# Kernel tuning notes

Hardware: AMD Instinct MI355X
Metric: run time of the kernel (lower is better)

## Reference

```python
import jax, jax.numpy as jnp
import numpy as np

B, T = 512, 200
N_SKILLS, M, DK, DV, H = 1000, 50, 64, 64, 128


def setup_inputs() -> dict:
    key = jax.random.key(0)
    ks = jax.random.split(key, 12)
    inp = {
        'skill_seq': jax.random.randint(ks[0], (B, T), 0, N_SKILLS, dtype=jnp.int32),
        'correct_seq': jax.random.randint(ks[1], (B, T), 0, 2, dtype=jnp.int32),
        'mask': jnp.ones((B, T), dtype=jnp.float32),
        'skill_embed': jax.random.normal(ks[2], (N_SKILLS, DK), dtype=jnp.float32),
        'key_memory': jax.random.normal(ks[3], (M, DK), dtype=jnp.float32) * 0.1,
        'value_init': jnp.zeros((M, DV), dtype=jnp.float32),
        'interaction_embed': jax.random.normal(ks[4], (2 * N_SKILLS, DV), dtype=jnp.float32),
        'erase_W': jax.random.normal(ks[5], (DV, DV), dtype=jnp.float32) * 0.05,
        'erase_b': jnp.zeros((DV,), dtype=jnp.float32),
        'add_W': jax.random.normal(ks[6], (DV, DV), dtype=jnp.float32) * 0.05,
        'add_b': jnp.zeros((DV,), dtype=jnp.float32),
        'fc1_W': jax.random.normal(ks[7], (DK + DV, H), dtype=jnp.float32) * 0.05,
        'fc1_b': jnp.zeros((H,), dtype=jnp.float32),
        'fc2_W': jax.random.normal(ks[8], (H, 1), dtype=jnp.float32) * 0.05,
        'fc2_b': jnp.zeros((1,), dtype=jnp.float32),
    }
    return inp


def reference(skill_seq, correct_seq, mask, skill_embed, key_memory, value_init,
              interaction_embed, erase_W, erase_b, add_W, add_b,
              fc1_W, fc1_b, fc2_W, fc2_b):
    n_skills = skill_embed.shape[0]
    b = skill_seq.shape[0]
    # Time-invariant-per-step quantities are precomputed vectorized over (B,T):
    q = skill_embed[skill_seq]                                   # (B,T,dk)
    w = jax.nn.softmax(jnp.einsum('btk,mk->btm', q, key_memory), axis=-1)  # (B,T,M)
    v = interaction_embed[skill_seq + correct_seq * n_skills]    # (B,T,dv)
    e = jax.nn.sigmoid(v @ erase_W + erase_b)                    # (B,T,dv)
    a = jnp.tanh(v @ add_W + add_b)                              # (B,T,dv)

    def step(mem, inputs):
        # mem: (B,M,dv); read BEFORE write, matching the torch loop
        w_t, e_t, a_t = inputs                                   # (B,M),(B,dv),(B,dv)
        read = jnp.einsum('bm,bmv->bv', w_t, mem)                # (B,dv)
        we = w_t[:, :, None]                                     # (B,M,1)
        mem = mem * (1.0 - we * e_t[:, None, :]) + we * a_t[:, None, :]
        return mem, read

    mem0 = jnp.broadcast_to(value_init, (b,) + value_init.shape)
    _, reads = jax.lax.scan(step, mem0,
                            (jnp.swapaxes(w, 0, 1), jnp.swapaxes(e, 0, 1), jnp.swapaxes(a, 0, 1)))
    reads = jnp.swapaxes(reads, 0, 1)                            # (B,T,dv)

    x = jnp.concatenate([q, reads], axis=-1)                     # (B,T,dk+dv)
    h = jax.nn.relu(x @ fc1_W + fc1_b)
    logit = (h @ fc2_W + fc2_b)[..., 0]
    p = jax.nn.sigmoid(logit)
    return p * mask, correct_seq.astype(jnp.float32) * mask
```

## Files before the change

### kernel.cpp

```cpp
#include <hip/hip_runtime.h>
#include <hip/hip_bf16.h>

#define B_  512
#define T_  200
#define NS  1000
#define M_  50
#define DK  64
#define DV  64
#define H_  128
#define NPOS (B_ * T_)

typedef __hip_bfloat16 bf16;
typedef unsigned short ushort_t;
typedef __bf16 bf16x8 __attribute__((ext_vector_type(8)));
typedef float  f32x4  __attribute__((ext_vector_type(4)));

__device__ __forceinline__ float ldf(const void* p, int i, int isbf) {
    return isbf ? __bfloat162float(((const bf16*)p)[i]) : ((const float*)p)[i];
}
__device__ __forceinline__ int sniff(const void* mask) {
    return (*(const unsigned*)mask == 0x3F800000u) ? 0 : 1;
}
__device__ __forceinline__ float rl(float x, int l) {
    return __int_as_float(__builtin_amdgcn_readlane(__float_as_int(x), l));
}
__device__ __forceinline__ ushort_t f2bf(float v) {
    bf16 h = __float2bfloat16(v);
    return *(ushort_t*)&h;
}

__global__ __launch_bounds__(256) void dk16_tabs(
    const void* __restrict__ mask,
    const void* __restrict__ skill_embed, const void* __restrict__ key_memory,
    const void* __restrict__ inter,
    const void* __restrict__ eW, const void* __restrict__ eb,
    const void* __restrict__ aW, const void* __restrict__ ab,
    const void* __restrict__ fc1W, const void* __restrict__ fc1b,
    float* __restrict__ w_tab, unsigned* __restrict__ ea_tab,
    float* __restrict__ hq_tab, ushort_t* __restrict__ W2f) {
    int isbf = sniff(mask);
    int lane = threadIdx.x & 63;
    int gwid = (blockIdx.x << 2) | (threadIdx.x >> 6);

    if (gwid < NS) {
        int s = gwid;
        float q = ldf(skill_embed, s * DK + lane, isbf);
        float acc = 0.f;
        if (lane < M_) {
            #pragma unroll 16
            for (int k = 0; k < DK; ++k)
                acc = fmaf(rl(q, k), ldf(key_memory, lane * DK + k, isbf), acc);
        }
        float val = (lane < M_) ? acc : -1e30f;
        float mx = val;
        #pragma unroll
        for (int off = 1; off < 64; off <<= 1) mx = fmaxf(mx, __shfl_xor(mx, off, 64));
        float ex = (lane < M_) ? __expf(val - mx) : 0.f;
        float sm = ex;
        #pragma unroll
        for (int off = 1; off < 64; off <<= 1) sm += __shfl_xor(sm, off, 64);
        w_tab[s * 64 + lane] = (lane < M_) ? ex / sm : 0.f;
    } else if (gwid < 3 * NS) {
        int r = gwid - NS;
        float vv = ldf(inter, r * DV + lane, isbf);
        float eacc = ldf(eb, lane, isbf);
        float aacc = ldf(ab, lane, isbf);
        #pragma unroll 16
        for (int u = 0; u < DV; ++u) {
            float vu = rl(vv, u);
            eacc = fmaf(vu, ldf(eW, u * DV + lane, isbf), eacc);
            aacc = fmaf(vu, ldf(aW, u * DV + lane, isbf), aacc);
        }
        float ev = 1.f / (1.f + __expf(-eacc));
        float av = tanhf(aacc);
        ea_tab[r * 64 + lane] = ((unsigned)f2bf(av) << 16) | (unsigned)f2bf(ev);
    } else if (gwid < 4 * NS) {
        int s = gwid - 3 * NS;
        float q = ldf(skill_embed, s * DK + lane, isbf);
        float acc0 = ldf(fc1b, lane, isbf);
        float acc1 = ldf(fc1b, 64 + lane, isbf);
        #pragma unroll 16
        for (int k = 0; k < DK; ++k) {
            float qk = rl(q, k);
            acc0 = fmaf(qk, ldf(fc1W, k * H_ + lane, isbf), acc0);
            acc1 = fmaf(qk, ldf(fc1W, k * H_ + 64 + lane, isbf), acc1);
        }
        hq_tab[s * H_ + lane]      = acc0;
        hq_tab[s * H_ + 64 + lane] = acc1;
    } else if (gwid < 4 * NS + 64) {
        int f = gwid - 4 * NS;
        int tile = f >> 3, kk = f & 7;
        int n = tile * 16 + (lane & 15);
        #pragma unroll
        for (int j = 0; j < 8; ++j) {
            int v = (kk * 32 + (lane >> 4) * 8 + j) & 63;
            W2f[(f * 64 + lane) * 8 + j] = f2bf(ldf(fc1W, (DK + v) * H_ + n, isbf));
        }
    }
}

template<int KS>
__global__ __launch_bounds__(64, 2) void dk16_scan(
    const int*  __restrict__ ss, const int* __restrict__ cs,
    const void* __restrict__ mask, const void* __restrict__ value_init,
    const float* __restrict__ w_tab, const unsigned* __restrict__ ea_tab,
    ushort_t* __restrict__ read_bf) {

    constexpr int NW = 16 / KS;
    int isbf = sniff(mask);
    int lane = threadIdx.x;
    int bk   = blockIdx.x;
    int b    = bk / KS, k = bk - b * KS;
    const int base = b * T_;
    const int row0 = (64 / KS) * k;
    const float4* w4 = (const float4*)w_tab;

    float4 mem[NW];
    #pragma unroll
    for (int i = 0; i < NW; ++i) {
        int r = row0 + 4 * i;
        mem[i].x = (r + 0 < M_) ? ldf(value_init, (r + 0) * DV + lane, isbf) : 0.f;
        mem[i].y = (r + 1 < M_) ? ldf(value_init, (r + 1) * DV + lane, isbf) : 0.f;
        mem[i].z = (r + 2 < M_) ? ldf(value_init, (r + 2) * DV + lane, isbf) : 0.f;
        mem[i].w = (r + 3 < M_) ? ldf(value_init, (r + 3) * DV + lane, isbf) : 0.f;
    }

    int s2 = ss[base + 2], c2 = cs[base + 2];
    int s3 = ss[base + 3], c3 = cs[base + 3];

    float4 wa[NW], wb[NW];
    unsigned eaA, eaB;
    {
        int sA = ss[base], cA = cs[base];
        eaA = ea_tab[(sA + cA * NS) * 64 + lane];
        #pragma unroll
        for (int i = 0; i < NW; ++i) wa[i] = w4[sA * 16 + NW * k + i];
        int sB = ss[base + 1], cB = cs[base + 1];
        eaB = ea_tab[(sB + cB * NS) * 64 + lane];
        #pragma unroll
        for (int i = 0; i < NW; ++i) wb[i] = w4[sB * 16 + NW * k + i];
    }

    for (int t = 0; t < T_; t += 2) {
        {
            float e0 = __uint_as_float(eaA << 16);
            float a0 = __uint_as_float(eaA & 0xFFFF0000u);
            float acc0 = 0.f, acc1 = 0.f, acc2 = 0.f, acc3 = 0.f;
            #pragma unroll
            for (int i = 0; i < NW; ++i) {
                float4 w = wa[i];
                acc0 = fmaf(w.x, mem[i].x, acc0);
                acc1 = fmaf(w.y, mem[i].y, acc1);
                acc2 = fmaf(w.z, mem[i].z, acc2);
                acc3 = fmaf(w.w, mem[i].w, acc3);
                mem[i].x = fmaf(-w.x, fmaf(e0, mem[i].x, -a0), mem[i].x);
                mem[i].y = fmaf(-w.y, fmaf(e0, mem[i].y, -a0), mem[i].y);
                mem[i].z = fmaf(-w.z, fmaf(e0, mem[i].z, -a0), mem[i].z);
                mem[i].w = fmaf(-w.w, fmaf(e0, mem[i].w, -a0), mem[i].w);
            }
            read_bf[((size_t)(base + t) * KS + k) * 64 + lane] =
                f2bf((acc0 + acc1) + (acc2 + acc3));
        }
        {
            eaA = ea_tab[(s2 + c2 * NS) * 64 + lane];
            #pragma unroll
            for (int i = 0; i < NW; ++i) wa[i] = w4[s2 * 16 + NW * k + i];
        }
        s2 = s3; c2 = c3;
        int tf = (t + 4 < T_) ? t + 4 : T_ - 1;
        s3 = ss[base + tf]; c3 = cs[base + tf];

        {
            float e1 = __uint_as_float(eaB << 16);
            float a1 = __uint_as_float(eaB & 0xFFFF0000u);
            float acc0 = 0.f, acc1 = 0.f, acc2 = 0.f, acc3 = 0.f;
            #pragma unroll
            for (int i = 0; i < NW; ++i) {
                float4 w = wb[i];
                acc0 = fmaf(w.x, mem[i].x, acc0);
                acc1 = fmaf(w.y, mem[i].y, acc1);
                acc2 = fmaf(w.z, mem[i].z, acc2);
                acc3 = fmaf(w.w, mem[i].w, acc3);
                mem[i].x = fmaf(-w.x, fmaf(e1, mem[i].x, -a1), mem[i].x);
                mem[i].y = fmaf(-w.y, fmaf(e1, mem[i].y, -a1), mem[i].y);
                mem[i].z = fmaf(-w.z, fmaf(e1, mem[i].z, -a1), mem[i].z);
                mem[i].w = fmaf(-w.w, fmaf(e1, mem[i].w, -a1), mem[i].w);
            }
            read_bf[((size_t)(base + t + 1) * KS + k) * 64 + lane] =
                f2bf((acc0 + acc1) + (acc2 + acc3));
        }
        {
            eaB = ea_tab[(s2 + c2 * NS) * 64 + lane];
            #pragma unroll
            for (int i = 0; i < NW; ++i) wb[i] = w4[s2 * 16 + NW * k + i];
        }
        s2 = s3; c2 = c3;
        tf = (t + 5 < T_) ? t + 5 : T_ - 1;
        s3 = ss[base + tf]; c3 = cs[base + tf];
    }
}

#define FOR8(X) X(0) X(1) X(2) X(3) X(4) X(5) X(6) X(7)
#define DECL_BT(t) bf16x8 b##t##_0, b##t##_1, b##t##_2, b##t##_3, \
                          b##t##_4, b##t##_5, b##t##_6, b##t##_7;
#define LOAD_BT(t) \
    b##t##_0 = B8[((t)*8+0)*64+lane]; b##t##_1 = B8[((t)*8+1)*64+lane]; \
    b##t##_2 = B8[((t)*8+2)*64+lane]; b##t##_3 = B8[((t)*8+3)*64+lane]; \
    b##t##_4 = B8[((t)*8+4)*64+lane]; b##t##_5 = B8[((t)*8+5)*64+lane]; \
    b##t##_6 = B8[((t)*8+6)*64+lane]; b##t##_7 = B8[((t)*8+7)*64+lane];
#define DECL_C(t)  f32x4 c##t = {0.f, 0.f, 0.f, 0.f};
#define LOAD_A(kk) bf16x8 a##kk = A8[col * 32 + (kk) * 4 + quad];
#define MFMA_KK(kk) \
    c0 = __builtin_amdgcn_mfma_f32_16x16x32_bf16(a##kk, b0_##kk, c0, 0, 0, 0); \
    c1 = __builtin_amdgcn_mfma_f32_16x16x32_bf16(a##kk, b1_##kk, c1, 0, 0, 0); \
    c2 = __builtin_amdgcn_mfma_f32_16x16x32_bf16(a##kk, b2_##kk, c2, 0, 0, 0); \
    c3 = __builtin_amdgcn_mfma_f32_16x16x32_bf16(a##kk, b3_##kk, c3, 0, 0, 0); \
    c4 = __builtin_amdgcn_mfma_f32_16x16x32_bf16(a##kk, b4_##kk, c4, 0, 0, 0); \
    c5 = __builtin_amdgcn_mfma_f32_16x16x32_bf16(a##kk, b5_##kk, c5, 0, 0, 0); \
    c6 = __builtin_amdgcn_mfma_f32_16x16x32_bf16(a##kk, b6_##kk, c6, 0, 0, 0); \
    c7 = __builtin_amdgcn_mfma_f32_16x16x32_bf16(a##kk, b7_##kk, c7, 0, 0, 0);
#define EPI(t) { \
    float h; \
    h = c##t.x + hq_tab[s0r * H_ + t * 16 + col]; x0 = fmaf(fmaxf(h, 0.f), f2w##t, x0); \
    h = c##t.y + hq_tab[s1r * H_ + t * 16 + col]; x1 = fmaf(fmaxf(h, 0.f), f2w##t, x1); \
    h = c##t.z + hq_tab[s2r * H_ + t * 16 + col]; x2 = fmaf(fmaxf(h, 0.f), f2w##t, x2); \
    h = c##t.w + hq_tab[s3r * H_ + t * 16 + col]; x3 = fmaf(fmaxf(h, 0.f), f2w##t, x3); }

__global__ __launch_bounds__(64)
__attribute__((amdgpu_waves_per_eu(1))) void dk16_fc4(
    const int*  __restrict__ skill_seq, const int* __restrict__ correct_seq,
    const void* __restrict__ mask,
    const void* __restrict__ fc2W, const void* __restrict__ fc2b,
    const float* __restrict__ hq_tab, const ushort_t* __restrict__ W2f,
    const ushort_t* __restrict__ read_bf,
    float* __restrict__ out0, float* __restrict__ out1) {

    int isbf = sniff(mask);
    int lane = threadIdx.x;
    int col  = lane & 15, quad = lane >> 4;

    const bf16x8* B8 = (const bf16x8*)W2f;
    DECL_BT(0) DECL_BT(1) DECL_BT(2) DECL_BT(3)
    DECL_BT(4) DECL_BT(5) DECL_BT(6) DECL_BT(7)
    FOR8(LOAD_BT)

    float f2w0 = ldf(fc2W,   0 + col, isbf), f2w1 = ldf(fc2W,  16 + col, isbf);
    float f2w2 = ldf(fc2W,  32 + col, isbf), f2w3 = ldf(fc2W,  48 + col, isbf);
    float f2w4 = ldf(fc2W,  64 + col, isbf), f2w5 = ldf(fc2W,  80 + col, isbf);
    float f2w6 = ldf(fc2W,  96 + col, isbf), f2w7 = ldf(fc2W, 112 + col, isbf);
    float f2b  = ldf(fc2b, 0, isbf);

    for (int pg = blockIdx.x; pg < NPOS / 16; pg += gridDim.x) {
        int p0 = pg * 16;
        const bf16x8* A8 = (const bf16x8*)(read_bf + (size_t)p0 * 256);
        LOAD_A(0) LOAD_A(1) LOAD_A(2) LOAD_A(3)
        LOAD_A(4) LOAD_A(5) LOAD_A(6) LOAD_A(7)

        int s0r = skill_seq[p0 + quad * 4 + 0];
        int s1r = skill_seq[p0 + quad * 4 + 1];
        int s2r = skill_seq[p0 + quad * 4 + 2];
        int s3r = skill_seq[p0 + quad * 4 + 3];

        FOR8(DECL_C)
        FOR8(MFMA_KK)

        float x0 = 0.f, x1 = 0.f, x2 = 0.f, x3 = 0.f;
        FOR8(EPI)

        #pragma unroll
        for (int off = 1; off < 16; off <<= 1) {
            x0 += __shfl_xor(x0, off, 64);
            x1 += __shfl_xor(x1, off, 64);
            x2 += __shfl_xor(x2, off, 64);
            x3 += __shfl_xor(x3, off, 64);
        }

        float mk0 = ldf(mask, p0 + quad * 4 + 0, isbf);
        float mk1 = ldf(mask, p0 + quad * 4 + 1, isbf);
        float mk2 = ldf(mask, p0 + quad * 4 + 2, isbf);
        float mk3 = ldf(mask, p0 + quad * 4 + 3, isbf);
        if (col == 0) {
            out0[p0 + quad * 4 + 0] = mk0 / (1.f + __expf(-(x0 + f2b)));
            out0[p0 + quad * 4 + 1] = mk1 / (1.f + __expf(-(x1 + f2b)));
            out0[p0 + quad * 4 + 2] = mk2 / (1.f + __expf(-(x2 + f2b)));
            out0[p0 + quad * 4 + 3] = mk3 / (1.f + __expf(-(x3 + f2b)));
        }
        if (col == 1) {
            out1[p0 + quad * 4 + 0] = (float)correct_seq[p0 + quad * 4 + 0] * mk0;
            out1[p0 + quad * 4 + 1] = (float)correct_seq[p0 + quad * 4 + 1] * mk1;
            out1[p0 + quad * 4 + 2] = (float)correct_seq[p0 + quad * 4 + 2] * mk2;
            out1[p0 + quad * 4 + 3] = (float)correct_seq[p0 + quad * 4 + 3] * mk3;
        }
    }
}

#define FCKK_G(kk) { \
    bf16x8 av = A8[col * (8 * KS) + (kk) * 4 + quad]; \
    c0 = __builtin_amdgcn_mfma_f32_16x16x32_bf16(av, B8[(0 * 8 + (kk)) * 64 + lane], c0, 0, 0, 0); \
    c1 = __builtin_amdgcn_mfma_f32_16x16x32_bf16(av, B8[(1 * 8 + (kk)) * 64 + lane], c1, 0, 0, 0); \
    c2 = __builtin_amdgcn_mfma_f32_16x16x32_bf16(av, B8[(2 * 8 + (kk)) * 64 + lane], c2, 0, 0, 0); \
    c3 = __builtin_amdgcn_mfma_f32_16x16x32_bf16(av, B8[(3 * 8 + (kk)) * 64 + lane], c3, 0, 0, 0); \
    c4 = __builtin_amdgcn_mfma_f32_16x16x32_bf16(av, B8[(4 * 8 + (kk)) * 64 + lane], c4, 0, 0, 0); \
    c5 = __builtin_amdgcn_mfma_f32_16x16x32_bf16(av, B8[(5 * 8 + (kk)) * 64 + lane], c5, 0, 0, 0); \
    c6 = __builtin_amdgcn_mfma_f32_16x16x32_bf16(av, B8[(6 * 8 + (kk)) * 64 + lane], c6, 0, 0, 0); \
    c7 = __builtin_amdgcn_mfma_f32_16x16x32_bf16(av, B8[(7 * 8 + (kk)) * 64 + lane], c7, 0, 0, 0); }

template<int KS>
__global__ __launch_bounds__(256) void dk16_fcgen(
    const int*  __restrict__ skill_seq, const int* __restrict__ correct_seq,
    const void* __restrict__ mask,
    const void* __restrict__ fc2W, const void* __restrict__ fc2b,
    const float* __restrict__ hq_tab, const ushort_t* __restrict__ W2f,
    const ushort_t* __restrict__ read_bf,
    float* __restrict__ out0, float* __restrict__ out1) {

    int isbf = sniff(mask);
    int lane = threadIdx.x & 63;
    int wid  = (blockIdx.x << 2) | (threadIdx.x >> 6);
    int p0   = wid * 16;
    int col  = lane & 15, quad = lane >> 4;

    const bf16x8* B8 = (const bf16x8*)W2f;
    const bf16x8* A8 = (const bf16x8*)(read_bf + (size_t)p0 * (64 * KS));

    FOR8(DECL_C)
    FCKK_G(0) FCKK_G(1) FCKK_G(2) FCKK_G(3)

    float f2w0 = ldf(fc2W,   0 + col, isbf), f2w1 = ldf(fc2W,  16 + col, isbf);
    float f2w2 = ldf(fc2W,  32 + col, isbf), f2w3 = ldf(fc2W,  48 + col, isbf);
    float f2w4 = ldf(fc2W,  64 + col, isbf), f2w5 = ldf(fc2W,  80 + col, isbf);
    float f2w6 = ldf(fc2W,  96 + col, isbf), f2w7 = ldf(fc2W, 112 + col, isbf);
    float f2b  = ldf(fc2b, 0, isbf);

    int s0r = skill_seq[p0 + quad * 4 + 0];
    int s1r = skill_seq[p0 + quad * 4 + 1];
    int s2r = skill_seq[p0 + quad * 4 + 2];
    int s3r = skill_seq[p0 + quad * 4 + 3];

    float x0 = 0.f, x1 = 0.f, x2 = 0.f, x3 = 0.f;
    FOR8(EPI)

    #pragma unroll
    for (int off = 1; off < 16; off <<= 1) {
        x0 += __shfl_xor(x0, off, 64);
        x1 += __shfl_xor(x1, off, 64);
        x2 += __shfl_xor(x2, off, 64);
        x3 += __shfl_xor(x3, off, 64);
    }

    float mk0 = ldf(mask, p0 + quad * 4 + 0, isbf);
    float mk1 = ldf(mask, p0 + quad * 4 + 1, isbf);
    float mk2 = ldf(mask, p0 + quad * 4 + 2, isbf);
    float mk3 = ldf(mask, p0 + quad * 4 + 3, isbf);
    if (col == 0) {
        out0[p0 + quad * 4 + 0] = mk0 / (1.f + __expf(-(x0 + f2b)));
        out0[p0 + quad * 4 + 1] = mk1 / (1.f + __expf(-(x1 + f2b)));
        out0[p0 + quad * 4 + 2] = mk2 / (1.f + __expf(-(x2 + f2b)));
        out0[p0 + quad * 4 + 3] = mk3 / (1.f + __expf(-(x3 + f2b)));
    }
    if (col == 1) {
        out1[p0 + quad * 4 + 0] = (float)correct_seq[p0 + quad * 4 + 0] * mk0;
        out1[p0 + quad * 4 + 1] = (float)correct_seq[p0 + quad * 4 + 1] * mk1;
        out1[p0 + quad * 4 + 2] = (float)correct_seq[p0 + quad * 4 + 2] * mk2;
        out1[p0 + quad * 4 + 3] = (float)correct_seq[p0 + quad * 4 + 3] * mk3;
    }
}

extern "C" void kernel_launch(void* const* d_in, const int* in_sizes, int n_in,
                              void* d_out, int out_size, void* d_ws, size_t ws_size,
                              hipStream_t stream) {
    const int*  skill_seq   = (const int*)d_in[0];
    const int*  correct_seq = (const int*)d_in[1];
    const void* mask        = d_in[2];
    const void* skill_embed = d_in[3];
    const void* key_memory  = d_in[4];
    const void* value_init  = d_in[5];
    const void* inter       = d_in[6];
    const void* erase_W     = d_in[7];
    const void* erase_b     = d_in[8];
    const void* add_W       = d_in[9];
    const void* add_b       = d_in[10];
    const void* fc1_W       = d_in[11];
    const void* fc1_b       = d_in[12];
    const void* fc2_W       = d_in[13];
    const void* fc2_b       = d_in[14];
    float* out = (float*)d_out;

    float*    ws      = (float*)d_ws + 16;
    float*    w_tab   = ws;
    unsigned* ea_tab  = (unsigned*)(ws + 64000);
    float*    hq_tab  = ws + 192000;
    ushort_t* W2f     = (ushort_t*)(ws + 320000);
    ushort_t* read_bf = (ushort_t*)(ws + 336400);

    dk16_tabs<<<1016, 256, 0, stream>>>(mask, skill_embed, key_memory, inter,
                                        erase_W, erase_b, add_W, add_b,
                                        fc1_W, fc1_b,
                                        w_tab, ea_tab, hq_tab, W2f);

    if (ws_size >= (size_t)54 * 1000 * 1000) {
        dk16_scan<4><<<B_ * 4, 64, 0, stream>>>(skill_seq, correct_seq, mask, value_init,
                                                w_tab, ea_tab, read_bf);
        dk16_fc4<<<1024, 64, 0, stream>>>(skill_seq, correct_seq, mask,
                                          fc2_W, fc2_b, hq_tab, W2f, read_bf,
                                          out, out + (size_t)NPOS);
    } else {
        dk16_scan<2><<<B_ * 2, 64, 0, stream>>>(skill_seq, correct_seq, mask, value_init,
                                                w_tab, ea_tab, read_bf);
        dk16_fcgen<2><<<1600, 256, 0, stream>>>(skill_seq, correct_seq, mask,
                                                fc2_W, fc2_b, hq_tab, W2f, read_bf,
                                                out, out + (size_t)NPOS);
    }
}
```

Baseline: 182.5 us.

## Deepen scan prefetch to four steps and double-buffer A loads in fc4

The KS=4 scan kernel becomes a dedicated version that keeps weight and erase/add rows for four future timesteps in registers, so the table loads for each step have more latency to hide behind the serial memory update. The fc4 kernel now software-pipelines the read_bf A-fragments, loading the next position group's operands while the current group's MFMAs and epilogue run, and its grid doubles to 2048 blocks. This raises register pressure in both kernels, which may reduce occupancy. The KS=2 path is only de-templated.

```diff
diff --git a/kernel.cpp b/kernel.cpp
--- a/kernel.cpp
+++ b/kernel.cpp
@@ -29,7 +29,7 @@
     return *(ushort_t*)&h;
 }
 
-__global__ __launch_bounds__(256) void dk16_tabs(
+__global__ __launch_bounds__(256) void dk18_tabs(
     const void* __restrict__ mask,
     const void* __restrict__ skill_embed, const void* __restrict__ key_memory,
     const void* __restrict__ inter,
@@ -99,20 +99,99 @@
     }
 }
 
-template<int KS>
-__global__ __launch_bounds__(64, 2) void dk16_scan(
+#define STEP4(S, tt) { \
+    float e0 = __uint_as_float(ea##S << 16); \
+    float a0 = __uint_as_float(ea##S & 0xFFFF0000u); \
+    float acc0 = 0.f, acc1 = 0.f, acc2 = 0.f, acc3 = 0.f; \
+    _Pragma("unroll") \
+    for (int i = 0; i < 4; ++i) { \
+        float4 w = w##S[i]; \
+        acc0 = fmaf(w.x, mem[i].x, acc0); \
+        acc1 = fmaf(w.y, mem[i].y, acc1); \
+        acc2 = fmaf(w.z, mem[i].z, acc2); \
+        acc3 = fmaf(w.w, mem[i].w, acc3); \
+        mem[i].x = fmaf(-w.x, fmaf(e0, mem[i].x, -a0), mem[i].x); \
+        mem[i].y = fmaf(-w.y, fmaf(e0, mem[i].y, -a0), mem[i].y); \
+        mem[i].z = fmaf(-w.z, fmaf(e0, mem[i].z, -a0), mem[i].z); \
+        mem[i].w = fmaf(-w.w, fmaf(e0, mem[i].w, -a0), mem[i].w); \
+    } \
+    read_bf[((size_t)(base + (tt)) * 4 + k) * 64 + lane] = \
+        f2bf((acc0 + acc1) + (acc2 + acc3)); }
+
+#define REFILL4(S, sx, cx) { \
+    ea##S = ea_tab[((sx) + (cx) * NS) * 64 + lane]; \
+    const float4* wp = w4 + (size_t)(sx) * 16 + 4 * k; \
+    _Pragma("unroll") \
+    for (int i = 0; i < 4; ++i) w##S[i] = wp[i]; }
+
+__global__ __launch_bounds__(64, 2) void dk18_scan4(
     const int*  __restrict__ ss, const int* __restrict__ cs,
     const void* __restrict__ mask, const void* __restrict__ value_init,
     const float* __restrict__ w_tab, const unsigned* __restrict__ ea_tab,
     ushort_t* __restrict__ read_bf) {
 
-    constexpr int NW = 16 / KS;
+    int isbf = sniff(mask);
+    int lane = threadIdx.x;
+    int bk   = blockIdx.x;
+    int b    = bk >> 2, k = bk & 3;
+    const int base = b * T_;
+    const int row0 = 16 * k;
+    const float4* w4 = (const float4*)w_tab;
+
+    float4 mem[4];
+    #pragma unroll
+    for (int i = 0; i < 4; ++i) {
+        int r = row0 + 4 * i;
+        mem[i].x = (r + 0 < M_) ? ldf(value_init, (r + 0) * DV + lane, isbf) : 0.f;
+        mem[i].y = (r + 1 < M_) ? ldf(value_init, (r + 1) * DV + lane, isbf) : 0.f;
+        mem[i].z = (r + 2 < M_) ? ldf(value_init, (r + 2) * DV + lane, isbf) : 0.f;
+        mem[i].w = (r + 3 < M_) ? ldf(value_init, (r + 3) * DV + lane, isbf) : 0.f;
+    }
+
+    float4 wA[4], wB[4], wC[4], wD[4];
+    unsigned eaA, eaB, eaC, eaD;
+    {
+        int s0 = ss[base + 0], c0 = cs[base + 0]; REFILL4(A, s0, c0)
+        int s1 = ss[base + 1], c1 = cs[base + 1]; REFILL4(B, s1, c1)
+        int s_2 = ss[base + 2], c_2 = cs[base + 2]; REFILL4(C, s_2, c_2)
+        int s_3 = ss[base + 3], c_3 = cs[base + 3]; REFILL4(D, s_3, c_3)
+    }
+    int sE = ss[base + 4], cE = cs[base + 4];
+    int sF = ss[base + 5], cF = cs[base + 5];
+
+    for (int t = 0; t < T_; t += 4) {
+        int tn;
+        STEP4(A, t + 0)
+        REFILL4(A, sE, cE)
+        tn = (t + 6 < T_) ? t + 6 : T_ - 1; sE = ss[base + tn]; cE = cs[base + tn];
+
+        STEP4(B, t + 1)
+        REFILL4(B, sF, cF)
+        tn = (t + 7 < T_) ? t + 7 : T_ - 1; sF = ss[base + tn]; cF = cs[base + tn];
+
+        STEP4(C, t + 2)
+        REFILL4(C, sE, cE)
+        tn = (t + 8 < T_) ? t + 8 : T_ - 1; sE = ss[base + tn]; cE = cs[base + tn];
+
+        STEP4(D, t + 3)
+        REFILL4(D, sF, cF)
+        tn = (t + 9 < T_) ? t + 9 : T_ - 1; sF = ss[base + tn]; cF = cs[base + tn];
+    }
+}
+
+__global__ __launch_bounds__(64, 2) void dk18_scan2(
+    const int*  __restrict__ ss, const int* __restrict__ cs,
+    const void* __restrict__ mask, const void* __restrict__ value_init,
+    const float* __restrict__ w_tab, const unsigned* __restrict__ ea_tab,
+    ushort_t* __restrict__ read_bf) {
+
+    constexpr int KS = 2, NW = 8;
     int isbf = sniff(mask);
     int lane = threadIdx.x;
     int bk   = blockIdx.x;
     int b    = bk / KS, k = bk - b * KS;
     const int base = b * T_;
-    const int row0 = (64 / KS) * k;
+    const int row0 = 32 * k;
     const float4* w4 = (const float4*)w_tab;
 
     float4 mem[NW];
@@ -127,7 +206,6 @@
 
     int s2 = ss[base + 2], c2 = cs[base + 2];
     int s3 = ss[base + 3], c3 = cs[base + 3];
-
     float4 wa[NW], wb[NW];
     unsigned eaA, eaB;
     {
@@ -169,7 +247,6 @@
         s2 = s3; c2 = c3;
         int tf = (t + 4 < T_) ? t + 4 : T_ - 1;
         s3 = ss[base + tf]; c3 = cs[base + tf];
-
         {
             float e1 = __uint_as_float(eaB << 16);
             float a1 = __uint_as_float(eaB & 0xFFFF0000u);
@@ -209,7 +286,6 @@
     b##t##_4 = B8[((t)*8+4)*64+lane]; b##t##_5 = B8[((t)*8+5)*64+lane]; \
     b##t##_6 = B8[((t)*8+6)*64+lane]; b##t##_7 = B8[((t)*8+7)*64+lane];
 #define DECL_C(t)  f32x4 c##t = {0.f, 0.f, 0.f, 0.f};
-#define LOAD_A(kk) bf16x8 a##kk = A8[col * 32 + (kk) * 4 + quad];
 #define MFMA_KK(kk) \
     c0 = __builtin_amdgcn_mfma_f32_16x16x32_bf16(a##kk, b0_##kk, c0, 0, 0, 0); \
     c1 = __builtin_amdgcn_mfma_f32_16x16x32_bf16(a##kk, b1_##kk, c1, 0, 0, 0); \
@@ -227,7 +303,7 @@
     h = c##t.w + hq_tab[s3r * H_ + t * 16 + col]; x3 = fmaf(fmaxf(h, 0.f), f2w##t, x3); }
 
 __global__ __launch_bounds__(64)
-__attribute__((amdgpu_waves_per_eu(1))) void dk16_fc4(
+__attribute__((amdgpu_waves_per_eu(1))) void dk18_fc4(
     const int*  __restrict__ skill_seq, const int* __restrict__ correct_seq,
     const void* __restrict__ mask,
     const void* __restrict__ fc2W, const void* __restrict__ fc2b,
@@ -250,11 +326,23 @@
     float f2w6 = ldf(fc2W,  96 + col, isbf), f2w7 = ldf(fc2W, 112 + col, isbf);
     float f2b  = ldf(fc2b, 0, isbf);
 
-    for (int pg = blockIdx.x; pg < NPOS / 16; pg += gridDim.x) {
+    const bf16x8* A8 = (const bf16x8*)(read_bf + (size_t)blockIdx.x * 16 * 256);
+    bf16x8 a0 = A8[col * 32 + 0 * 4 + quad], a1 = A8[col * 32 + 1 * 4 + quad];
+    bf16x8 a2 = A8[col * 32 + 2 * 4 + quad], a3 = A8[col * 32 + 3 * 4 + quad];
+    bf16x8 a4 = A8[col * 32 + 4 * 4 + quad], a5 = A8[col * 32 + 5 * 4 + quad];
+    bf16x8 a6 = A8[col * 32 + 6 * 4 + quad], a7 = A8[col * 32 + 7 * 4 + quad];
+
+    for (int pg = blockIdx.x; pg < NPOS / 16; pg += 2048) {
         int p0 = pg * 16;
-        const bf16x8* A8 = (const bf16x8*)(read_bf + (size_t)p0 * 256);
-        LOAD_A(0) LOAD_A(1) LOAD_A(2) LOAD_A(3)
-        LOAD_A(4) LOAD_A(5) LOAD_A(6) LOAD_A(7)
+        int png = pg + 2048;
+        bf16x8 n0, n1, n2, n3, n4, n5, n6, n7;
+        if (png < NPOS / 16) {
+            const bf16x8* AN = (const bf16x8*)(read_bf + (size_t)png * 16 * 256);
+            n0 = AN[col * 32 + 0 * 4 + quad]; n1 = AN[col * 32 + 1 * 4 + quad];
+            n2 = AN[col * 32 + 2 * 4 + quad]; n3 = AN[col * 32 + 3 * 4 + quad];
+            n4 = AN[col * 32 + 4 * 4 + quad]; n5 = AN[col * 32 + 5 * 4 + quad];
+            n6 = AN[col * 32 + 6 * 4 + quad]; n7 = AN[col * 32 + 7 * 4 + quad];
+        }
 
         int s0r = skill_seq[p0 + quad * 4 + 0];
         int s1r = skill_seq[p0 + quad * 4 + 1];
@@ -262,7 +350,8 @@
         int s3r = skill_seq[p0 + quad * 4 + 3];
 
         FOR8(DECL_C)
-        FOR8(MFMA_KK)
+        MFMA_KK(0) MFMA_KK(1) MFMA_KK(2) MFMA_KK(3)
+        MFMA_KK(4) MFMA_KK(5) MFMA_KK(6) MFMA_KK(7)
 
         float x0 = 0.f, x1 = 0.f, x2 = 0.f, x3 = 0.f;
         FOR8(EPI)
@@ -291,11 +380,13 @@
             out1[p0 + quad * 4 + 2] = (float)correct_seq[p0 + quad * 4 + 2] * mk2;
             out1[p0 + quad * 4 + 3] = (float)correct_seq[p0 + quad * 4 + 3] * mk3;
         }
+        a0 = n0; a1 = n1; a2 = n2; a3 = n3;
+        a4 = n4; a5 = n5; a6 = n6; a7 = n7;
     }
 }
 
 #define FCKK_G(kk) { \
-    bf16x8 av = A8[col * (8 * KS) + (kk) * 4 + quad]; \
+    bf16x8 av = A8[col * 16 + (kk) * 4 + quad]; \
     c0 = __builtin_amdgcn_mfma_f32_16x16x32_bf16(av, B8[(0 * 8 + (kk)) * 64 + lane], c0, 0, 0, 0); \
     c1 = __builtin_amdgcn_mfma_f32_16x16x32_bf16(av, B8[(1 * 8 + (kk)) * 64 + lane], c1, 0, 0, 0); \
     c2 = __builtin_amdgcn_mfma_f32_16x16x32_bf16(av, B8[(2 * 8 + (kk)) * 64 + lane], c2, 0, 0, 0); \
@@ -305,8 +396,7 @@
     c6 = __builtin_amdgcn_mfma_f32_16x16x32_bf16(av, B8[(6 * 8 + (kk)) * 64 + lane], c6, 0, 0, 0); \
     c7 = __builtin_amdgcn_mfma_f32_16x16x32_bf16(av, B8[(7 * 8 + (kk)) * 64 + lane], c7, 0, 0, 0); }
 
-template<int KS>
-__global__ __launch_bounds__(256) void dk16_fcgen(
+__global__ __launch_bounds__(256) void dk18_fc2(
     const int*  __restrict__ skill_seq, const int* __restrict__ correct_seq,
     const void* __restrict__ mask,
     const void* __restrict__ fc2W, const void* __restrict__ fc2b,
@@ -321,7 +411,7 @@
     int col  = lane & 15, quad = lane >> 4;
 
     const bf16x8* B8 = (const bf16x8*)W2f;
-    const bf16x8* A8 = (const bf16x8*)(read_bf + (size_t)p0 * (64 * KS));
+    const bf16x8* A8 = (const bf16x8*)(read_bf + (size_t)p0 * 128);
 
     FOR8(DECL_C)
     FCKK_G(0) FCKK_G(1) FCKK_G(2) FCKK_G(3)
@@ -393,22 +483,22 @@
     ushort_t* W2f     = (ushort_t*)(ws + 320000);
     ushort_t* read_bf = (ushort_t*)(ws + 336400);
 
-    dk16_tabs<<<1016, 256, 0, stream>>>(mask, skill_embed, key_memory, inter,
+    dk18_tabs<<<1016, 256, 0, stream>>>(mask, skill_embed, key_memory, inter,
                                         erase_W, erase_b, add_W, add_b,
                                         fc1_W, fc1_b,
                                         w_tab, ea_tab, hq_tab, W2f);
 
     if (ws_size >= (size_t)54 * 1000 * 1000) {
-        dk16_scan<4><<<B_ * 4, 64, 0, stream>>>(skill_seq, correct_seq, mask, value_init,
-                                                w_tab, ea_tab, read_bf);
-        dk16_fc4<<<1024, 64, 0, stream>>>(skill_seq, correct_seq, mask,
+        dk18_scan4<<<B_ * 4, 64, 0, stream>>>(skill_seq, correct_seq, mask, value_init,
+                                              w_tab, ea_tab, read_bf);
+        dk18_fc4<<<2048, 64, 0, stream>>>(skill_seq, correct_seq, mask,
                                           fc2_W, fc2_b, hq_tab, W2f, read_bf,
                                           out, out + (size_t)NPOS);
     } else {
-        dk16_scan<2><<<B_ * 2, 64, 0, stream>>>(skill_seq, correct_seq, mask, value_init,
-                                                w_tab, ea_tab, read_bf);
-        dk16_fcgen<2><<<1600, 256, 0, stream>>>(skill_seq, correct_seq, mask,
-                                                fc2_W, fc2_b, hq_tab, W2f, read_bf,
-                                                out, out + (size_t)NPOS);
-    }
-}
+        dk18_scan2<<<B_ * 2, 64, 0, stream>>>(skill_seq, correct_seq, mask, value_init,
+                                              w_tab, ea_tab, read_bf);
+        dk18_fc2<<<1600, 256, 0, stream>>>(skill_seq, correct_seq, mask,
+                                           fc2_W, fc2_b, hq_tab, W2f, read_bf,
+                                           out, out + (size_t)NPOS);
+    }
+}
```

After: 220.9 us. 1.21x slower.
